# Optimization experiments

Hardware: AMD Instinct MI355X
Metric: run time of the kernel (lower is better)

Reference implementation:

```python
import jax, jax.numpy as jnp
import numpy as np

N_NODES = 100000
N_EDGES = 1600000
IN_DIM = 128
HID = 128


def setup_inputs() -> dict:
    key = jax.random.key(0)
    ks = jax.random.split(key, 8)
    x = jax.random.normal(ks[0], (N_NODES, IN_DIM), dtype=jnp.float32)
    edge_index = jax.random.randint(ks[1], (2, N_EDGES), 0, N_NODES, dtype=jnp.int32)
    s = 1.0 / np.sqrt(IN_DIM)
    # layer 1: in_dim -> hidden; layer 2: hidden -> hidden
    Wl1 = jax.random.uniform(ks[2], (IN_DIM, HID), jnp.float32, -s, s)
    bl1 = jnp.zeros((HID,), jnp.float32)
    Wr1 = jax.random.uniform(ks[3], (IN_DIM, HID), jnp.float32, -s, s)
    s2 = 1.0 / np.sqrt(HID)
    Wl2 = jax.random.uniform(ks[4], (HID, HID), jnp.float32, -s2, s2)
    bl2 = jnp.zeros((HID,), jnp.float32)
    Wr2 = jax.random.uniform(ks[5], (HID, HID), jnp.float32, -s2, s2)
    return {"x": x, "edge_index": edge_index, "Wl1": Wl1, "bl1": bl1, "Wr1": Wr1,
            "Wl2": Wl2, "bl2": bl2, "Wr2": Wr2}


def _sage_conv(h, src, dst, Wl, bl, Wr, n_nodes):
    # mean aggregation of neighbor (source) features at destination nodes
    msg = h[src]                                               # [E, D] gather
    agg = jax.ops.segment_sum(msg, dst, num_segments=n_nodes)  # [N, D]
    deg = jax.ops.segment_sum(jnp.ones((src.shape[0],), h.dtype), dst,
                              num_segments=n_nodes)            # [N]
    agg = agg / jnp.maximum(deg, 1.0)[:, None]
    # PyG SAGEConv: lin_l(aggregated) + lin_r(root); lin_r has no bias
    return agg @ Wl + bl + h @ Wr


def reference(x, edge_index, Wl1, bl1, Wr1, Wl2, bl2, Wr2):
    src, dst = edge_index[0], edge_index[1]
    n = x.shape[0]
    h = jax.nn.relu(_sage_conv(x, src, dst, Wl1, bl1, Wr1, n))
    # dropout is identity in eval mode
    h = jax.nn.relu(_sage_conv(h, src, dst, Wl2, bl2, Wr2, n))
    return h
```

## Files before the change

### kernel.cpp

```cpp
#include <hip/hip_runtime.h>
#include <stdint.h>

#define DIM 128

typedef __attribute__((ext_vector_type(8))) short short8;
typedef __attribute__((ext_vector_type(4))) float floatx4;
typedef __attribute__((ext_vector_type(2))) float floatx2;

__device__ __forceinline__ unsigned short f2bf(float f){
  union { float f; unsigned int i; } c; c.f = f;
  unsigned int u = c.i;
  return (unsigned short)((u + 0x7fffu + ((u >> 16) & 1u)) >> 16);
}
__device__ __forceinline__ float up_lo(unsigned int v){ return __uint_as_float(v << 16); }
__device__ __forceinline__ float up_hi(unsigned int v){ return __uint_as_float(v & 0xffff0000u); }


__global__ __launch_bounds__(256) void k_prep(const float* __restrict__ in,
    unsigned short* __restrict__ out, int n4,
    const int* __restrict__ dst, int E, int* __restrict__ bktCnt){
  __shared__ int h[256];
  h[threadIdx.x] = 0;
  __syncthreads();
  int i = blockIdx.x * 256 + threadIdx.x;
  int stride = gridDim.x * 256;
  for (int k = i; k < n4; k += stride){
    float4 v = ((const float4*)in)[k];
    ushort4 o;
    o.x = f2bf(v.x); o.y = f2bf(v.y); o.z = f2bf(v.z); o.w = f2bf(v.w);
    ((ushort4*)out)[k] = o;
  }
  for (int k = i; k < E; k += stride) atomicAdd(&h[dst[k] >> 9], 1);
  __syncthreads();
  int v = h[threadIdx.x];
  if (v) atomicAdd(&bktCnt[threadIdx.x], v);
}


__global__ __launch_bounds__(256) void k_hist(const int* __restrict__ dst, int E,
                                              int* __restrict__ deg){
  int e = blockIdx.x * 256 + threadIdx.x;
  if (e < E) atomicAdd(&deg[dst[e]], 1);
}

__global__ __launch_bounds__(256) void k_scan1(const int* __restrict__ deg, int N,
    int* __restrict__ out, int* __restrict__ bsum){
  __shared__ int sd[256];
  int t = threadIdx.x;
  int base = blockIdx.x * 1024 + t * 4;
  int v0=0, v1=0, v2=0, v3=0;
  if (base + 3 < N) { int4 q = *(const int4*)(deg + base); v0=q.x; v1=q.y; v2=q.z; v3=q.w; }
  else {
    if (base + 0 < N) v0 = deg[base + 0];
    if (base + 1 < N) v1 = deg[base + 1];
    if (base + 2 < N) v2 = deg[base + 2];
  }
  int s = v0 + v1 + v2 + v3;
  sd[t] = s;
  __syncthreads();
  #pragma unroll
  for (int off = 1; off < 256; off <<= 1){
    int x = (t >= off) ? sd[t - off] : 0;
    __syncthreads();
    sd[t] += x;
    __syncthreads();
  }
  int inc = sd[t];
  int exc = inc - s;
  if (base + 0 < N) out[base + 0] = exc;
  if (base + 1 < N) out[base + 1] = exc + v0;
  if (base + 2 < N) out[base + 2] = exc + v0 + v1;
  if (base + 3 < N) out[base + 3] = exc + v0 + v1 + v2;
  if (t == 255) bsum[blockIdx.x] = inc;
}

__global__ __launch_bounds__(128) void k_scan2(int* __restrict__ bsum, int nb){
  __shared__ int sd[128];
  int t = threadIdx.x;
  int v = (t < nb) ? bsum[t] : 0;
  sd[t] = v;
  __syncthreads();
  #pragma unroll
  for (int off = 1; off < 128; off <<= 1){
    int x = (t >= off) ? sd[t - off] : 0;
    __syncthreads();
    sd[t] += x;
    __syncthreads();
  }
  if (t < nb) bsum[t] = sd[t] - v;
}

__global__ __launch_bounds__(256) void k_scan3(int* __restrict__ rowptr,
    const int* __restrict__ bsum, int N, int E, int* __restrict__ cursor){
  int i = blockIdx.x * 256 + threadIdx.x;
  if (i < N){
    int v = rowptr[i] + bsum[i >> 10];
    rowptr[i] = v;
    cursor[i] = v;
  }
  if (i == 0) rowptr[N] = E;
}

__global__ __launch_bounds__(256) void k_fill(const int* __restrict__ src,
    const int* __restrict__ dst, int E, int* __restrict__ cursor, int* __restrict__ col){
  int e = blockIdx.x * 256 + threadIdx.x;
  if (e < E){
    int d = dst[e];
    int pos = atomicAdd(&cursor[d], 1);
    col[pos] = src[e];
  }
}


#define BINCH 2048

__global__ __launch_bounds__(256) void k_bin(const int* __restrict__ src,
    const int* __restrict__ dst, int E,
    const int* __restrict__ bktCnt, int* __restrict__ cursor,
    int2* __restrict__ binned, int NB){
  __shared__ int2 buf[BINCH];
  __shared__ unsigned char bidArr[BINCH];
  __shared__ int cnt[256], startA[256], gstart[256], gbase[256];
  int t = threadIdx.x;
  int bc = bktCnt[t];
  cnt[t] = bc;
  __syncthreads();
  #pragma unroll
  for (int off = 1; off < 256; off <<= 1){
    int x = (t >= off) ? cnt[t - off] : 0;
    __syncthreads();
    cnt[t] += x;
    __syncthreads();
  }
  gbase[t] = cnt[t] - bc;
  __syncthreads();
  cnt[t] = 0;
  __syncthreads();
  int base = blockIdx.x * BINCH;
  int s_[8], d_[8], r_[8];
  #pragma unroll
  for (int i = 0; i < 8; ++i){
    int e = base + i * 256 + t;
    bool v = (e < E);
    s_[i] = v ? src[e] : 0;
    d_[i] = v ? dst[e] : -1;
    r_[i] = v ? atomicAdd(&cnt[d_[i] >> 9], 1) : 0;
  }
  __syncthreads();
  int v = cnt[t];
  startA[t] = v;
  __syncthreads();
  #pragma unroll
  for (int off = 1; off < 256; off <<= 1){
    int y = (t >= off) ? startA[t - off] : 0;
    __syncthreads();
    startA[t] += y;
    __syncthreads();
  }
  int incl = startA[t];
  __syncthreads();
  startA[t] = incl - v;
  __syncthreads();
  #pragma unroll
  for (int i = 0; i < 8; ++i){
    if (d_[i] >= 0){
      int b = d_[i] >> 9;
      int slot = startA[b] + r_[i];
      buf[slot] = make_int2(s_[i], d_[i]);
      bidArr[slot] = (unsigned char)b;
    }
  }
  if (cnt[t] > 0) gstart[t] = atomicAdd(&cursor[t], cnt[t]);
  __syncthreads();
  int total = startA[255] + cnt[255];
  for (int j = t; j < total; j += 256){
    int b = bidArr[j];
    binned[gbase[b] + gstart[b] + (j - startA[b])] = buf[j];
  }
}


__global__ __launch_bounds__(1024) void k_csr2(const int2* __restrict__ binned,
    const int* __restrict__ bktCnt, int N, int* __restrict__ rowptr,
    int* __restrict__ col){
  __shared__ int cnt[512], excl[512], cur[512];
  __shared__ int sd[256];
  __shared__ int s_lo, s_hi;
  int b = blockIdx.x;
  int node0 = b << 9;
  int nNodes = min(512, N - node0);
  int t = threadIdx.x;
  if (t < 256) sd[t] = bktCnt[t];
  __syncthreads();
  #pragma unroll
  for (int off = 1; off < 256; off <<= 1){
    int x = 0;
    if (t < 256 && t >= off) x = sd[t - off];
    __syncthreads();
    if (t < 256) sd[t] += x;
    __syncthreads();
  }
  if (t == 0){ s_hi = sd[b]; s_lo = sd[b] - bktCnt[b]; }
  if (t < 512){ cnt[t] = 0; cur[t] = 0; }
  __syncthreads();
  int lo = s_lo, hi = s_hi;
  for (int e = lo + t; e < hi; e += 1024)
    atomicAdd(&cnt[binned[e].y - node0], 1);
  __syncthreads();
  int c0 = 0, c1 = 0, ps = 0;
  if (t < 256){
    c0 = cnt[2 * t]; c1 = cnt[2 * t + 1];
    ps = c0 + c1;
    sd[t] = ps;
  }
  __syncthreads();
  #pragma unroll
  for (int off = 1; off < 256; off <<= 1){
    int x = 0;
    if (t < 256 && t >= off) x = sd[t - off];
    __syncthreads();
    if (t < 256) sd[t] += x;
    __syncthreads();
  }
  if (t < 256){
    int pexcl = sd[t] - ps;
    excl[2 * t] = pexcl;
    excl[2 * t + 1] = pexcl + c0;
  }
  __syncthreads();
  for (int j = t; j < nNodes; j += 1024) rowptr[node0 + j] = lo + excl[j];
  if (t == 0) rowptr[node0 + nNodes] = hi;
  for (int e = lo + t; e < hi; e += 1024){
    int2 pr = binned[e];
    int dl = pr.y - node0;
    int loc = atomicAdd(&cur[dl], 1);
    col[lo + excl[dl] + loc] = pr.x;
  }
}


__device__ __forceinline__ void acc8(floatx2* a, uint4 u){
  a[0] += (floatx2){up_lo(u.x), up_hi(u.x)};
  a[1] += (floatx2){up_lo(u.y), up_hi(u.y)};
  a[2] += (floatx2){up_lo(u.z), up_hi(u.z)};
  a[3] += (floatx2){up_lo(u.w), up_hi(u.w)};
}

__global__ __launch_bounds__(256) void k_agg_bf(const unsigned short* __restrict__ feat,
    const int* __restrict__ rowptr, const int* __restrict__ col,
    unsigned short* __restrict__ out, int N){
  int wid = (blockIdx.x * 256 + threadIdx.x) >> 6;
  if (wid >= N) return;
  int lane = threadIdx.x & 63;
  int q = lane >> 4, s = lane & 15;
  int beg = rowptr[wid], end = rowptr[wid + 1];
  int deg = end - beg;
  floatx2 av[4];
  #pragma unroll
  for (int i = 0; i < 4; ++i) av[i] = (floatx2){0.f, 0.f};

  int myIdx = (beg + lane < end) ? col[beg + lane] : 0;

  int o0 = q, o1 = 4 + q, o2 = 8 + q, o3 = 12 + q;
  int n0 = __shfl(myIdx, o0, 64);
  int n1 = __shfl(myIdx, o1, 64);
  int n2 = __shfl(myIdx, o2, 64);
  int n3 = __shfl(myIdx, o3, 64);
  uint4 u0 = ((const uint4*)(feat + (size_t)n0 * DIM))[s];
  uint4 u1 = ((const uint4*)(feat + (size_t)n1 * DIM))[s];
  uint4 u2 = ((const uint4*)(feat + (size_t)n2 * DIM))[s];
  uint4 u3 = ((const uint4*)(feat + (size_t)n3 * DIM))[s];

  bool g1 = deg > 16;
  int o4 = 16 + q, o5 = 20 + q, o6 = 24 + q, o7 = 28 + q;
  uint4 u4, u5, u6, u7;
  if (g1){
    int n4 = __shfl(myIdx, o4, 64);
    int n5 = __shfl(myIdx, o5, 64);
    int n6 = __shfl(myIdx, o6, 64);
    int n7 = __shfl(myIdx, o7, 64);
    u4 = ((const uint4*)(feat + (size_t)n4 * DIM))[s];
    u5 = ((const uint4*)(feat + (size_t)n5 * DIM))[s];
    u6 = ((const uint4*)(feat + (size_t)n6 * DIM))[s];
    u7 = ((const uint4*)(feat + (size_t)n7 * DIM))[s];
  }

  if (o0 < deg) acc8(av, u0);
  if (o1 < deg) acc8(av, u1);
  if (o2 < deg) acc8(av, u2);
  if (o3 < deg) acc8(av, u3);
  if (g1){
    if (o4 < deg) acc8(av, u4);
    if (o5 < deg) acc8(av, u5);
    if (o6 < deg) acc8(av, u6);
    if (o7 < deg) acc8(av, u7);
  }

  for (int e = beg + 32; e < end; e += 16){
    int i0 = e + q, i1 = e + 4 + q, i2 = e + 8 + q, i3 = e + 12 + q;
    int m0 = col[i0 < end ? i0 : beg];
    int m1 = col[i1 < end ? i1 : beg];
    int m2 = col[i2 < end ? i2 : beg];
    int m3 = col[i3 < end ? i3 : beg];
    uint4 v0 = ((const uint4*)(feat + (size_t)m0 * DIM))[s];
    uint4 v1 = ((const uint4*)(feat + (size_t)m1 * DIM))[s];
    uint4 v2 = ((const uint4*)(feat + (size_t)m2 * DIM))[s];
    uint4 v3 = ((const uint4*)(feat + (size_t)m3 * DIM))[s];
    if (i0 < end) acc8(av, v0);
    if (i1 < end) acc8(av, v1);
    if (i2 < end) acc8(av, v2);
    if (i3 < end) acc8(av, v3);
  }

  float a[8];
  #pragma unroll
  for (int i = 0; i < 4; ++i){ a[2 * i] = av[i][0]; a[2 * i + 1] = av[i][1]; }

  #pragma unroll
  for (int i = 0; i < 8; ++i){
    a[i] += __shfl_xor(a[i], 16, 64);
    a[i] += __shfl_xor(a[i], 32, 64);
  }
  if (q == 0){
    int d = deg;
    float r = 1.0f / (float)(d > 1 ? d : 1);
    uint4 o;
    o.x = (unsigned int)f2bf(a[0] * r) | ((unsigned int)f2bf(a[1] * r) << 16);
    o.y = (unsigned int)f2bf(a[2] * r) | ((unsigned int)f2bf(a[3] * r) << 16);
    o.z = (unsigned int)f2bf(a[4] * r) | ((unsigned int)f2bf(a[5] * r) << 16);
    o.w = (unsigned int)f2bf(a[6] * r) | ((unsigned int)f2bf(a[7] * r) << 16);
    ((uint4*)(out + (size_t)wid * DIM))[s] = o;
  }
}


__global__ __launch_bounds__(256) void k_agg_f32(const float* __restrict__ feat,
    const int* __restrict__ rowptr, const int* __restrict__ col,
    unsigned short* __restrict__ out, int N){
  int wid = (blockIdx.x * 256 + threadIdx.x) >> 6;
  if (wid >= N) return;
  int lane = threadIdx.x & 63;
  int beg = rowptr[wid], end = rowptr[wid + 1];
  float a0 = 0.f, a1 = 0.f;
  int off = lane * 2;
  int e = beg;
  for (; e + 4 <= end; e += 4){
    int s0 = col[e], s1 = col[e+1], s2 = col[e+2], s3 = col[e+3];
    float2 v0 = *(const float2*)(feat + (size_t)s0 * DIM + off);
    float2 v1 = *(const float2*)(feat + (size_t)s1 * DIM + off);
    float2 v2 = *(const float2*)(feat + (size_t)s2 * DIM + off);
    float2 v3 = *(const float2*)(feat + (size_t)s3 * DIM + off);
    a0 += v0.x + v1.x + v2.x + v3.x;
    a1 += v0.y + v1.y + v2.y + v3.y;
  }
  for (; e < end; ++e){
    float2 v = *(const float2*)(feat + (size_t)col[e] * DIM + off);
    a0 += v.x; a1 += v.y;
  }
  int d = end - beg;
  float r = 1.0f / (float)(d > 1 ? d : 1);
  a0 *= r; a1 *= r;
  unsigned int o = (unsigned int)f2bf(a0) | ((unsigned int)f2bf(a1) << 16);
  *(unsigned int*)(out + (size_t)wid * DIM + off) = o;
}


template<bool OUTBF>
__global__ __launch_bounds__(256, 2) void k_gemm_r(const unsigned short* __restrict__ A1,
    const unsigned short* __restrict__ A2,
    const float* __restrict__ Wl, const float* __restrict__ Wr,
    const float* __restrict__ bias,
    float* __restrict__ outf, unsigned short* __restrict__ outb, int M)
{
  int lane = threadIdx.x & 63;
  int c = lane & 15, quad = lane >> 4;
  int gwid = blockIdx.x * 4 + (threadIdx.x >> 6);
  int nwaves = gridDim.x * 4;
  int half = gwid & 1;
  int colbase = half * 64;

  short8 B[2][4][4];
  #pragma unroll
  for (int w = 0; w < 2; ++w){
    const float* W = w ? Wr : Wl;
    #pragma unroll
    for (int km = 0; km < 4; ++km){
      #pragma unroll
      for (int j = 0; j < 4; ++j){
        union { short8 v; unsigned short u[8]; } tb;
        #pragma unroll
        for (int i = 0; i < 8; ++i)
          tb.u[i] = f2bf(W[(km * 32 + quad * 8 + i) * 128 + colbase + j * 16 + c]);
        B[w][km][j] = tb.v;
      }
    }
  }
  float bv[4];
  #pragma unroll
  for (int j = 0; j < 4; ++j) bv[j] = bias[colbase + j * 16 + c];

  int ntasks = M >> 4;
  int stride = nwaves >> 1;
  int task = gwid >> 1;
  short8 a1[4], a2[4];
  if (task < ntasks){
    const unsigned short* ap1 = A1 + (size_t)((task << 4) + c) * DIM + quad * 8;
    const unsigned short* ap2 = A2 + (size_t)((task << 4) + c) * DIM + quad * 8;
    #pragma unroll
    for (int km = 0; km < 4; ++km){
      a1[km] = *(const short8*)(ap1 + km * 32);
      a2[km] = *(const short8*)(ap2 + km * 32);
    }
  }
  for (; task < ntasks; task += stride){
    int nxt = task + stride;
    int pt = nxt < ntasks ? nxt : task;
    const unsigned short* p1 = A1 + (size_t)((pt << 4) + c) * DIM + quad * 8;
    const unsigned short* p2 = A2 + (size_t)((pt << 4) + c) * DIM + quad * 8;
    short8 n1[4], n2[4];
    #pragma unroll
    for (int km = 0; km < 4; ++km){
      n1[km] = *(const short8*)(p1 + km * 32);
      n2[km] = *(const short8*)(p2 + km * 32);
    }
    floatx4 acc[4];
    #pragma unroll
    for (int j = 0; j < 4; ++j) acc[j] = (floatx4){0.f, 0.f, 0.f, 0.f};
    #pragma unroll
    for (int km = 0; km < 4; ++km){
      #pragma unroll
      for (int j = 0; j < 4; ++j){
        acc[j] = __builtin_amdgcn_mfma_f32_16x16x32_bf16(a1[km], B[0][km][j], acc[j], 0, 0, 0);
        acc[j] = __builtin_amdgcn_mfma_f32_16x16x32_bf16(a2[km], B[1][km][j], acc[j], 0, 0, 0);
      }
    }
    int row0 = task << 4;
    #pragma unroll
    for (int j = 0; j < 4; ++j){
      int colIdx = colbase + j * 16 + c;
      #pragma unroll
      for (int r = 0; r < 4; ++r){
        int row = row0 + quad * 4 + r;
        float v = fmaxf(acc[j][r] + bv[j], 0.f);
        if (OUTBF) outb[(size_t)row * DIM + colIdx] = f2bf(v);
        else       outf[(size_t)row * DIM + colIdx] = v;
      }
    }
    #pragma unroll
    for (int km = 0; km < 4; ++km){ a1[km] = n1[km]; a2[km] = n2[km]; }
  }
}


__global__ __launch_bounds__(256) void k_gemm_f(const unsigned short* __restrict__ A1,
    const float* __restrict__ A2f,
    const float* __restrict__ Wl, const float* __restrict__ Wr,
    const float* __restrict__ bias, float* __restrict__ outf, int M)
{
  __shared__ unsigned short lds[2 * 128 * 128];
  for (int h = threadIdx.x; h < 128 * 128; h += 256){
    int k = h >> 7, n = h & 127;
    int idx = n * 128 + ((((k >> 3) ^ (n & 7)) << 3)) + (k & 7);
    lds[idx]         = f2bf(Wl[h]);
    lds[16384 + idx] = f2bf(Wr[h]);
  }
  __syncthreads();
  int lane = threadIdx.x & 63;
  int c = lane & 15, quad = lane >> 4;
  int gwid = blockIdx.x * 4 + (threadIdx.x >> 6);
  int nwaves = gridDim.x * 4;
  int ntasks = M >> 4;
  for (int task = gwid; task < ntasks; task += nwaves){
    int row0 = task << 4;
    floatx4 acc[8];
    #pragma unroll
    for (int j = 0; j < 8; ++j) acc[j] = (floatx4){0.f, 0.f, 0.f, 0.f};
    const unsigned short* ap1 = A1 + (size_t)(row0 + c) * DIM + quad * 8;
    #pragma unroll
    for (int km = 0; km < 4; ++km){
      short8 a = *(const short8*)(ap1 + km * 32);
      int kb = (km << 2) + quad;
      #pragma unroll
      for (int j = 0; j < 8; ++j){
        short8 b = *(const short8*)(&lds[(j * 16 + c) * 128 + ((kb ^ (c & 7)) << 3)]);
        acc[j] = __builtin_amdgcn_mfma_f32_16x16x32_bf16(a, b, acc[j], 0, 0, 0);
      }
    }
    #pragma unroll
    for (int km = 0; km < 4; ++km){
      const float* ap2 = A2f + (size_t)(row0 + c) * DIM + quad * 8;
      float4 p0 = *(const float4*)(ap2 + km * 32);
      float4 p1 = *(const float4*)(ap2 + km * 32 + 4);
      union { short8 v; unsigned short u[8]; } ua;
      ua.u[0] = f2bf(p0.x); ua.u[1] = f2bf(p0.y);
      ua.u[2] = f2bf(p0.z); ua.u[3] = f2bf(p0.w);
      ua.u[4] = f2bf(p1.x); ua.u[5] = f2bf(p1.y);
      ua.u[6] = f2bf(p1.z); ua.u[7] = f2bf(p1.w);
      int kb = (km << 2) + quad;
      #pragma unroll
      for (int j = 0; j < 8; ++j){
        short8 b = *(const short8*)(&lds[16384 + (j * 16 + c) * 128 + ((kb ^ (c & 7)) << 3)]);
        acc[j] = __builtin_amdgcn_mfma_f32_16x16x32_bf16(ua.v, b, acc[j], 0, 0, 0);
      }
    }
    #pragma unroll
    for (int j = 0; j < 8; ++j){
      int colIdx = j * 16 + c;
      float bvv = bias[colIdx];
      #pragma unroll
      for (int r = 0; r < 4; ++r){
        int row = row0 + quad * 4 + r;
        outf[(size_t)row * DIM + colIdx] = fmaxf(acc[j][r] + bvv, 0.f);
      }
    }
  }
}


extern "C" void kernel_launch(void* const* d_in, const int* in_sizes, int n_in,
                              void* d_out, int out_size, void* d_ws, size_t ws_size,
                              hipStream_t stream)
{
  const float* x   = (const float*)d_in[0];
  const int*   ei  = (const int*)d_in[1];
  const float* Wl1 = (const float*)d_in[2];
  const float* bl1 = (const float*)d_in[3];
  const float* Wr1 = (const float*)d_in[4];
  const float* Wl2 = (const float*)d_in[5];
  const float* bl2 = (const float*)d_in[6];
  const float* Wr2 = (const float*)d_in[7];

  const int N = in_sizes[0] / DIM;
  const int E = in_sizes[1] / 2;
  const int* src  = ei;
  const int* dstI = ei + E;
  const int NB = (N + 511) >> 9;

  char* p = (char*)d_ws;
  auto alloc = [&](size_t bytes) -> char* {
    char* r = p; p += (bytes + 255) & ~((size_t)255); return r;
  };
  int* rowptr   = (int*)alloc((size_t)(N + 1) * 4);
  int* deg      = (int*)alloc((size_t)N * 4);
  int* bsum     = (int*)alloc(1024);
  int* bktCnt   = (int*)alloc(1024);
  int* bktCur   = (int*)alloc(1024);
  int* col      = (int*)alloc((size_t)E * 4);
  unsigned short* aggb = (unsigned short*)alloc((size_t)N * DIM * 2);
  unsigned short* xb   = (unsigned short*)alloc((size_t)N * DIM * 2);
  unsigned short* h1b  = (unsigned short*)alloc((size_t)N * DIM * 2);
  size_t need_big = (size_t)(p - (char*)d_ws);
  const bool big = (ws_size >= need_big) && (NB <= 255);
  int2* binned = (int2*)aggb;

  int gE = (E + 255) / 256;
  int gAgg = (N * 64 + 255) / 256;

  if (big){
    int n4 = N * DIM / 4;
    hipMemsetAsync(bktCnt, 0, 2048, stream);
    k_prep<<<1024, 256, 0, stream>>>(x, xb, n4, dstI, E, bktCnt);
    k_bin<<<(E + BINCH - 1) / BINCH, 256, 0, stream>>>(src, dstI, E, bktCnt, bktCur,
                                                       binned, NB);
    k_csr2<<<NB, 1024, 0, stream>>>(binned, bktCnt, N, rowptr, col);
    k_agg_bf<<<gAgg, 256, 0, stream>>>(xb, rowptr, col, aggb, N);
    k_gemm_r<true><<<512, 256, 0, stream>>>(aggb, xb, Wl1, Wr1, bl1,
                                            nullptr, h1b, N);
    k_agg_bf<<<gAgg, 256, 0, stream>>>(h1b, rowptr, col, aggb, N);
    k_gemm_r<false><<<512, 256, 0, stream>>>(aggb, h1b, Wl2, Wr2, bl2,
                                             (float*)d_out, nullptr, N);
  } else {
    hipMemsetAsync(deg, 0, (size_t)N * 4, stream);
    k_hist<<<gE, 256, 0, stream>>>(dstI, E, deg);
    int nb = (N + 1023) / 1024;
    k_scan1<<<nb, 256, 0, stream>>>(deg, N, rowptr, bsum);
    k_scan2<<<1, 128, 0, stream>>>(bsum, nb);
    k_scan3<<<(N + 255) / 256, 256, 0, stream>>>(rowptr, bsum, N, E, deg);
    k_fill<<<gE, 256, 0, stream>>>(src, dstI, E, deg, col);
    float* h1 = (float*)d_out;
    k_agg_f32<<<gAgg, 256, 0, stream>>>(x, rowptr, col, aggb, N);
    k_gemm_f<<<512, 256, 0, stream>>>(aggb, x, Wl1, Wr1, bl1, h1, N);
    k_agg_f32<<<gAgg, 256, 0, stream>>>(h1, rowptr, col, aggb, N);
    k_gemm_f<<<512, 256, 0, stream>>>(aggb, h1, Wl2, Wr2, bl2, (float*)d_out, N);
  }
}
```

Baseline: 332.9 us.

## Replace binned two-pass CSR build with atomic histogram, scan and fill

Removes the bucketed binning and per-bucket CSR kernels and instead computes per-node degree with global atomics fused into the bf16 conversion kernel, followed by a three-kernel prefix scan and an atomic scatter fill. This simplifies the construction and drops the bucket-count limit. In exchange it adds kernel launches and heavy global atomic contention, and the neighbor order within rows becomes nondeterministic.

```diff
diff --git a/kernel.cpp b/kernel.cpp
--- a/kernel.cpp
+++ b/kernel.cpp
@@ -16,12 +16,9 @@
 __device__ __forceinline__ float up_hi(unsigned int v){ return __uint_as_float(v & 0xffff0000u); }
 
 
-__global__ __launch_bounds__(256) void k_prep(const float* __restrict__ in,
+__global__ __launch_bounds__(256) void k_prep2(const float* __restrict__ in,
     unsigned short* __restrict__ out, int n4,
-    const int* __restrict__ dst, int E, int* __restrict__ bktCnt){
-  __shared__ int h[256];
-  h[threadIdx.x] = 0;
-  __syncthreads();
+    const int* __restrict__ dst, int E, int* __restrict__ deg){
   int i = blockIdx.x * 256 + threadIdx.x;
   int stride = gridDim.x * 256;
   for (int k = i; k < n4; k += stride){
@@ -30,10 +27,7 @@
     o.x = f2bf(v.x); o.y = f2bf(v.y); o.z = f2bf(v.z); o.w = f2bf(v.w);
     ((ushort4*)out)[k] = o;
   }
-  for (int k = i; k < E; k += stride) atomicAdd(&h[dst[k] >> 9], 1);
-  __syncthreads();
-  int v = h[threadIdx.x];
-  if (v) atomicAdd(&bktCnt[threadIdx.x], v);
+  for (int k = i; k < E; k += stride) atomicAdd(&deg[dst[k]], 1);
 }
 
 
@@ -108,133 +102,6 @@
     int d = dst[e];
     int pos = atomicAdd(&cursor[d], 1);
     col[pos] = src[e];
-  }
-}
-
-
-#define BINCH 2048
-
-__global__ __launch_bounds__(256) void k_bin(const int* __restrict__ src,
-    const int* __restrict__ dst, int E,
-    const int* __restrict__ bktCnt, int* __restrict__ cursor,
-    int2* __restrict__ binned, int NB){
-  __shared__ int2 buf[BINCH];
-  __shared__ unsigned char bidArr[BINCH];
-  __shared__ int cnt[256], startA[256], gstart[256], gbase[256];
-  int t = threadIdx.x;
-  int bc = bktCnt[t];
-  cnt[t] = bc;
-  __syncthreads();
-  #pragma unroll
-  for (int off = 1; off < 256; off <<= 1){
-    int x = (t >= off) ? cnt[t - off] : 0;
-    __syncthreads();
-    cnt[t] += x;
-    __syncthreads();
-  }
-  gbase[t] = cnt[t] - bc;
-  __syncthreads();
-  cnt[t] = 0;
-  __syncthreads();
-  int base = blockIdx.x * BINCH;
-  int s_[8], d_[8], r_[8];
-  #pragma unroll
-  for (int i = 0; i < 8; ++i){
-    int e = base + i * 256 + t;
-    bool v = (e < E);
-    s_[i] = v ? src[e] : 0;
-    d_[i] = v ? dst[e] : -1;
-    r_[i] = v ? atomicAdd(&cnt[d_[i] >> 9], 1) : 0;
-  }
-  __syncthreads();
-  int v = cnt[t];
-  startA[t] = v;
-  __syncthreads();
-  #pragma unroll
-  for (int off = 1; off < 256; off <<= 1){
-    int y = (t >= off) ? startA[t - off] : 0;
-    __syncthreads();
-    startA[t] += y;
-    __syncthreads();
-  }
-  int incl = startA[t];
-  __syncthreads();
-  startA[t] = incl - v;
-  __syncthreads();
-  #pragma unroll
-  for (int i = 0; i < 8; ++i){
-    if (d_[i] >= 0){
-      int b = d_[i] >> 9;
-      int slot = startA[b] + r_[i];
-      buf[slot] = make_int2(s_[i], d_[i]);
-      bidArr[slot] = (unsigned char)b;
-    }
-  }
-  if (cnt[t] > 0) gstart[t] = atomicAdd(&cursor[t], cnt[t]);
-  __syncthreads();
-  int total = startA[255] + cnt[255];
-  for (int j = t; j < total; j += 256){
-    int b = bidArr[j];
-    binned[gbase[b] + gstart[b] + (j - startA[b])] = buf[j];
-  }
-}
-
-
-__global__ __launch_bounds__(1024) void k_csr2(const int2* __restrict__ binned,
-    const int* __restrict__ bktCnt, int N, int* __restrict__ rowptr,
-    int* __restrict__ col){
-  __shared__ int cnt[512], excl[512], cur[512];
-  __shared__ int sd[256];
-  __shared__ int s_lo, s_hi;
-  int b = blockIdx.x;
-  int node0 = b << 9;
-  int nNodes = min(512, N - node0);
-  int t = threadIdx.x;
-  if (t < 256) sd[t] = bktCnt[t];
-  __syncthreads();
-  #pragma unroll
-  for (int off = 1; off < 256; off <<= 1){
-    int x = 0;
-    if (t < 256 && t >= off) x = sd[t - off];
-    __syncthreads();
-    if (t < 256) sd[t] += x;
-    __syncthreads();
-  }
-  if (t == 0){ s_hi = sd[b]; s_lo = sd[b] - bktCnt[b]; }
-  if (t < 512){ cnt[t] = 0; cur[t] = 0; }
-  __syncthreads();
-  int lo = s_lo, hi = s_hi;
-  for (int e = lo + t; e < hi; e += 1024)
-    atomicAdd(&cnt[binned[e].y - node0], 1);
-  __syncthreads();
-  int c0 = 0, c1 = 0, ps = 0;
-  if (t < 256){
-    c0 = cnt[2 * t]; c1 = cnt[2 * t + 1];
-    ps = c0 + c1;
-    sd[t] = ps;
-  }
-  __syncthreads();
-  #pragma unroll
-  for (int off = 1; off < 256; off <<= 1){
-    int x = 0;
-    if (t < 256 && t >= off) x = sd[t - off];
-    __syncthreads();
-    if (t < 256) sd[t] += x;
-    __syncthreads();
-  }
-  if (t < 256){
-    int pexcl = sd[t] - ps;
-    excl[2 * t] = pexcl;
-    excl[2 * t + 1] = pexcl + c0;
-  }
-  __syncthreads();
-  for (int j = t; j < nNodes; j += 1024) rowptr[node0 + j] = lo + excl[j];
-  if (t == 0) rowptr[node0 + nNodes] = hi;
-  for (int e = lo + t; e < hi; e += 1024){
-    int2 pr = binned[e];
-    int dl = pr.y - node0;
-    int loc = atomicAdd(&cur[dl], 1);
-    col[lo + excl[dl] + loc] = pr.x;
   }
 }
 
@@ -534,7 +401,6 @@
   const int E = in_sizes[1] / 2;
   const int* src  = ei;
   const int* dstI = ei + E;
-  const int NB = (N + 511) >> 9;
 
   char* p = (char*)d_ws;
   auto alloc = [&](size_t bytes) -> char* {
@@ -543,26 +409,25 @@
   int* rowptr   = (int*)alloc((size_t)(N + 1) * 4);
   int* deg      = (int*)alloc((size_t)N * 4);
   int* bsum     = (int*)alloc(1024);
-  int* bktCnt   = (int*)alloc(1024);
-  int* bktCur   = (int*)alloc(1024);
   int* col      = (int*)alloc((size_t)E * 4);
   unsigned short* aggb = (unsigned short*)alloc((size_t)N * DIM * 2);
   unsigned short* xb   = (unsigned short*)alloc((size_t)N * DIM * 2);
   unsigned short* h1b  = (unsigned short*)alloc((size_t)N * DIM * 2);
   size_t need_big = (size_t)(p - (char*)d_ws);
-  const bool big = (ws_size >= need_big) && (NB <= 255);
-  int2* binned = (int2*)aggb;
+  const bool big = (ws_size >= need_big);
 
   int gE = (E + 255) / 256;
   int gAgg = (N * 64 + 255) / 256;
+  int nb = (N + 1023) / 1024;
 
   if (big){
     int n4 = N * DIM / 4;
-    hipMemsetAsync(bktCnt, 0, 2048, stream);
-    k_prep<<<1024, 256, 0, stream>>>(x, xb, n4, dstI, E, bktCnt);
-    k_bin<<<(E + BINCH - 1) / BINCH, 256, 0, stream>>>(src, dstI, E, bktCnt, bktCur,
-                                                       binned, NB);
-    k_csr2<<<NB, 1024, 0, stream>>>(binned, bktCnt, N, rowptr, col);
+    hipMemsetAsync(deg, 0, (size_t)N * 4, stream);
+    k_prep2<<<1024, 256, 0, stream>>>(x, xb, n4, dstI, E, deg);
+    k_scan1<<<nb, 256, 0, stream>>>(deg, N, rowptr, bsum);
+    k_scan2<<<1, 128, 0, stream>>>(bsum, nb);
+    k_scan3<<<(N + 255) / 256, 256, 0, stream>>>(rowptr, bsum, N, E, deg);
+    k_fill<<<gE, 256, 0, stream>>>(src, dstI, E, deg, col);
     k_agg_bf<<<gAgg, 256, 0, stream>>>(xb, rowptr, col, aggb, N);
     k_gemm_r<true><<<512, 256, 0, stream>>>(aggb, xb, Wl1, Wr1, bl1,
                                             nullptr, h1b, N);
@@ -572,7 +437,6 @@
   } else {
     hipMemsetAsync(deg, 0, (size_t)N * 4, stream);
     k_hist<<<gE, 256, 0, stream>>>(dstI, E, deg);
-    int nb = (N + 1023) / 1024;
     k_scan1<<<nb, 256, 0, stream>>>(deg, N, rowptr, bsum);
     k_scan2<<<1, 128, 0, stream>>>(bsum, nb);
     k_scan3<<<(N + 255) / 256, 256, 0, stream>>>(rowptr, bsum, N, E, deg);
```

After: 459.8 us. 38.1% more time.
